# Kernel tuning notes

Hardware: AMD Instinct MI355X
Metric: run time of the kernel (lower is better)

## Reference

```python
import jax, jax.numpy as jnp
import numpy as np

N, E, G = 20000, 100000, 32
HID, HEADS, HC = 64, 8, 64  # hidden, heads, per-head channels (PyG: out_channels per head)
L, K = 3, 4


def setup_inputs() -> dict:
    key = jax.random.key(0)
    ks = jax.random.split(key, 20)
    rn = lambda k, s, sc=0.05: jax.random.normal(k, s, jnp.float32) * sc
    HO = HEADS * HC  # 512
    return {
        "x": jax.random.uniform(ks[0], (N, 7), jnp.float32),
        "edge_attr": jax.random.normal(ks[1], (E, 4), jnp.float32),
        "means": jax.random.normal(ks[2], (K, 8), jnp.float32),
        "log_stds": jnp.zeros((K, 8), jnp.float32),
        "sp_W": rn(ks[3], (K, HID), 0.3), "sp_b": jnp.zeros((HID,), jnp.float32),
        "ne_W": rn(ks[4], (7, HID), 0.3), "ne_b": jnp.zeros((HID,), jnp.float32),
        "ee_W": rn(ks[5], (4, HID), 0.3), "ee_b": jnp.zeros((HID,), jnp.float32),
        "Wq": rn(ks[6], (L, HID, HO)), "bq": jnp.zeros((L, HO), jnp.float32),
        "Wk": rn(ks[7], (L, HID, HO)), "bk": jnp.zeros((L, HO), jnp.float32),
        "Wv": rn(ks[8], (L, HID, HO)), "bv": jnp.zeros((L, HO), jnp.float32),
        "We": rn(ks[9], (L, HID, HO)), "be": jnp.zeros((L, HO), jnp.float32),
        "Ws": rn(ks[10], (L, HID, HID)), "bs": jnp.zeros((L, HID), jnp.float32),
        "eu_W": rn(ks[11], (L, 3 * HID, HID)), "eu_b": jnp.zeros((L, HID), jnp.float32),
        "rW1": rn(ks[12], (2 * HID, HID)), "rb1": jnp.zeros((HID,), jnp.float32),
        "rW2": rn(ks[13], (HID, HID)), "rb2": jnp.zeros((HID,), jnp.float32),
        "rW3": rn(ks[14], (HID, 2)), "rb3": jnp.zeros((2,), jnp.float32),
        "edge_index": jax.random.randint(ks[15], (2, E), 0, N, jnp.int32),
        "batch": jnp.sort(jax.random.randint(ks[16], (N,), 0, G, jnp.int32)),
        "num_graphs": G,
    }


def reference(x, edge_attr, means, log_stds, sp_W, sp_b, ne_W, ne_b, ee_W, ee_b,
              Wq, bq, Wk, bk, Wv, bv, We, be, Ws, bs, eu_W, eu_b,
              rW1, rb1, rW2, rb2, rW3, rb3, edge_index, batch, num_graphs):
    n = x.shape[0]
    src, dst = edge_index[0], edge_index[1]

    # ---- SpatialGaussianEncoder (dropout is identity in eval) ----
    p = x[:, :4]
    sl, sr = p[src, :2], p[src, 2:4]
    dl, dr = p[dst, :2], p[dst, 2:4]
    rel = jnp.stack([dl - sl, dl - sr, dr - sl, dr - sr], axis=1)  # [E,4,2]
    dist = jnp.linalg.norm(rel, axis=-1)                           # [E,4]
    ang = jnp.arctan2(rel[..., 1], rel[..., 0])                    # [E,4]
    u = jnp.stack([dist, ang], axis=-1).reshape(-1, 8)             # [E,8] (d,a)x4
    std = jnp.exp(log_stds) + 1e-6                                 # [K,8]
    z = (u[:, None, :] - means[None]) / std[None]                  # [E,K,8]
    w = jnp.exp(-0.5 * jnp.sum(z * z, axis=-1))                    # [E,K]
    sp = jax.nn.relu(w @ sp_W + sp_b)                              # [E,HID]

    h = jax.nn.relu(x @ ne_W + ne_b)                               # [N,HID]
    ea = jax.nn.relu(edge_attr @ ee_W + ee_b) + sp                 # [E,HID]

    scale = 1.0 / float(np.sqrt(HC))
    for l in range(L):
        # PyG TransformerConv(hidden, hidden, heads=8, edge_dim=hidden, concat=False)
        q = (h @ Wq[l] + bq[l]).reshape(n, HEADS, HC)
        k = (h @ Wk[l] + bk[l]).reshape(n, HEADS, HC)
        v = (h @ Wv[l] + bv[l]).reshape(n, HEADS, HC)
        e = (ea @ We[l] + be[l]).reshape(-1, HEADS, HC)
        kj = k[src] + e                                            # [E,H,C]
        alpha = jnp.einsum('ehc,ehc->eh', q[dst], kj) * scale      # [E,H]
        m = jax.ops.segment_max(alpha, dst, num_segments=n)
        ex = jnp.exp(alpha - m[dst])
        den = jax.ops.segment_sum(ex, dst, num_segments=n)
        a = ex / (den[dst] + 1e-16)                                # scatter-softmax over dst
        msg = a[:, :, None] * (v[src] + e)                         # [E,H,C]
        out = jax.ops.segment_sum(msg, dst, num_segments=n).mean(axis=1)  # concat=False -> head mean
        h = jax.nn.relu(out + h @ Ws[l] + bs[l])                   # skip (root_weight) + F.relu
        ef = jnp.concatenate([h[src], h[dst], ea], axis=1)         # [E,3*HID]
        ea = jax.nn.relu(ef @ eu_W[l] + eu_b[l])

    # ---- per-graph masked-mean pooling == segment mean ----
    cn = jnp.maximum(jax.ops.segment_sum(jnp.ones((n,), x.dtype), batch, num_segments=num_graphs), 1.0)
    node_pool = jax.ops.segment_sum(h, batch, num_segments=num_graphs) / cn[:, None]
    eb = batch[src]
    ce = jnp.maximum(jax.ops.segment_sum(jnp.ones((src.shape[0],), x.dtype), eb, num_segments=num_graphs), 1.0)
    edge_pool = jax.ops.segment_sum(ea, eb, num_segments=num_graphs) / ce[:, None]
    g = jnp.concatenate([node_pool, edge_pool], axis=1)            # [G,2*HID]

    h1 = jax.nn.relu(g @ rW1 + rb1)
    h2 = jax.nn.relu(h1 @ rW2 + rb2)
    return jnp.tanh(h2 @ rW3 + rb3)                                # [G,2]
```

## Files before the change

### kernel.cpp

```cpp
#include <hip/hip_runtime.h>
#include <hip/hip_bf16.h>
#include <cstdint>
#include <cstddef>



__global__ void __launch_bounds__(256) k_node_embed(
    const float* __restrict__ x, const float* __restrict__ neW, const float* __restrict__ neb,
    float* __restrict__ h, int N)
{
    int idx = blockIdx.x * 256 + threadIdx.x;
    int n = idx >> 6, c = idx & 63;
    if (n >= N) return;
    float acc = neb[c];
    #pragma unroll
    for (int j = 0; j < 7; ++j) acc += x[(size_t)n * 7 + j] * neW[j * 64 + c];
    h[(size_t)n * 64 + c] = fmaxf(acc, 0.f);
}

__global__ void __launch_bounds__(256) k_edge_w(
    const float* __restrict__ x,
    const float* __restrict__ means, const float* __restrict__ log_stds,
    const int* __restrict__ src, const int* __restrict__ dst,
    float* __restrict__ wbuf, int E)
{
    int e = blockIdx.x * 256 + threadIdx.x;
    if (e >= E) return;
    int s = src[e], d = dst[e];
    const float* ps = x + (size_t)s * 7;
    const float* pd = x + (size_t)d * 7;
    float slx = ps[0], sly = ps[1], srx = ps[2], sry = ps[3];
    float dlx = pd[0], dly = pd[1], drx = pd[2], dry = pd[3];
    float u[8];
    float rx, ry;
    rx = dlx - slx; ry = dly - sly; u[0] = sqrtf(rx*rx + ry*ry); u[1] = atan2f(ry, rx);
    rx = dlx - srx; ry = dly - sry; u[2] = sqrtf(rx*rx + ry*ry); u[3] = atan2f(ry, rx);
    rx = drx - slx; ry = dry - sly; u[4] = sqrtf(rx*rx + ry*ry); u[5] = atan2f(ry, rx);
    rx = drx - srx; ry = dry - sry; u[6] = sqrtf(rx*rx + ry*ry); u[7] = atan2f(ry, rx);
    #pragma unroll
    for (int kk = 0; kk < 4; ++kk) {
        float ssum = 0.f;
        #pragma unroll
        for (int dd = 0; dd < 8; ++dd) {
            float stdv = expf(log_stds[kk*8+dd]) + 1e-6f;
            float z = (u[dd] - means[kk*8+dd]) / stdv;
            ssum += z * z;
        }
        wbuf[(size_t)e*4 + kk] = expf(-0.5f * ssum);
    }
}

__global__ void __launch_bounds__(256) k_edge_ea(
    const float* __restrict__ edge_attr, const float* __restrict__ wbuf,
    const float* __restrict__ spW, const float* __restrict__ spb,
    const float* __restrict__ eeW, const float* __restrict__ eeb,
    float* __restrict__ ea, int E)
{
    int idx = blockIdx.x * 256 + threadIdx.x;
    int e = idx >> 6, c = idx & 63;
    if (e >= E) return;
    float acce = eeb[c];
    #pragma unroll
    for (int j = 0; j < 4; ++j) acce += edge_attr[(size_t)e*4 + j] * eeW[j*64 + c];
    float accs = spb[c];
    #pragma unroll
    for (int j = 0; j < 4; ++j) accs += wbuf[(size_t)e*4 + j] * spW[j*64 + c];
    ea[(size_t)e*64 + c] = fmaxf(acce, 0.f) + fmaxf(accs, 0.f);
}


__global__ void __launch_bounds__(256) k_hist(
    const int* __restrict__ dst, int* __restrict__ deg, int E)
{
    int e = blockIdx.x * 256 + threadIdx.x;
    if (e < E) atomicAdd(deg + dst[e], 1);
}

__global__ void __launch_bounds__(1024) k_scan(
    const int* __restrict__ deg, int* __restrict__ ptr, int* __restrict__ headw, int N)
{
    __shared__ int part[1024];
    int t = threadIdx.x;
    int per = (N + 1023) / 1024;
    int s = 0;
    for (int i = 0; i < per; ++i) { int idx = t*per + i; if (idx < N) s += deg[idx]; }
    part[t] = s;
    __syncthreads();
    for (int off = 1; off < 1024; off <<= 1) {
        int v = (t >= off) ? part[t - off] : 0;
        __syncthreads();
        part[t] += v;
        __syncthreads();
    }
    int base = (t > 0) ? part[t - 1] : 0;
    for (int i = 0; i < per; ++i) {
        int idx = t*per + i;
        if (idx < N) { ptr[idx] = base; headw[idx] = base; base += deg[idx]; }
    }
    if (t == 1023) ptr[N] = part[1023];
}

__global__ void __launch_bounds__(256) k_scatter(
    const int* __restrict__ dst, const int* __restrict__ src, const int* __restrict__ batch,
    int* __restrict__ headw, int2* __restrict__ ipair, int* __restrict__ ieb, int E)
{
    int e = blockIdx.x * 256 + threadIdx.x;
    if (e < E) {
        int s = src[e];
        int pos = atomicAdd(headw + dst[e], 1);
        ipair[pos] = make_int2(s, e);
        ieb[e] = batch[s];
    }
}


__global__ void __launch_bounds__(256) k_wprod_all(
    const float* __restrict__ Wq, const float* __restrict__ bq,
    const float* __restrict__ Wk, const float* __restrict__ We,
    float* __restrict__ Mk, float* __restrict__ Me,
    float* __restrict__ bqk, float* __restrict__ bqe)
{
    int h = blockIdx.x;
    int which = blockIdx.y;
    int l = blockIdx.z;
    const float* Wq_l = Wq + (size_t)l * 64 * 512;
    const float* bq_l = bq + (size_t)l * 512;
    const float* Wx_l = (which ? We : Wk) + (size_t)l * 64 * 512;
    float* M  = (which ? Me : Mk) + (size_t)l * 64 * 512;
    float* bM = (which ? bqe : bqk) + (size_t)l * 512;
    __shared__ float wq_s[65][64];
    __shared__ float wx_s[64][65];
    int tid = threadIdx.x;
    for (int i = tid; i < 4096; i += 256) {
        int r = i >> 6, c2 = i & 63;
        wq_s[r][c2] = Wq_l[(size_t)r*512 + h*64 + c2];
        wx_s[r][c2] = Wx_l[(size_t)r*512 + h*64 + c2];
    }
    if (tid < 64) wq_s[64][tid] = bq_l[h*64 + tid];
    __syncthreads();
    int j = tid & 63, cg = tid >> 6;
    for (int c = cg*16; c < cg*16 + 16; ++c) {
        float s = 0.f;
        #pragma unroll 8
        for (int c2 = 0; c2 < 64; ++c2) s += wq_s[c][c2] * wx_s[j][c2];
        M[(size_t)c*512 + h*64 + j] = s;
    }
    if (tid < 64) {
        float s = 0.f;
        #pragma unroll 8
        for (int c2 = 0; c2 < 64; ++c2) s += wq_s[64][c2] * wx_s[tid][c2];
        bM[h*64 + tid] = s;
    }
}

__global__ void __launch_bounds__(64) k_wqb_all(
    const float* __restrict__ Wq, const float* __restrict__ bq,
    const float* __restrict__ bk, const float* __restrict__ be,
    float* __restrict__ wqb, float* __restrict__ cb)
{
    int l = blockIdx.x;
    const float* Wq_l = Wq + (size_t)l * 64 * 512;
    const float* bq_l = bq + (size_t)l * 512;
    const float* bk_l = bk + (size_t)l * 512;
    const float* be_l = be + (size_t)l * 512;
    float* wqb_l = wqb + (size_t)l * 512;
    float* cb_l  = cb + (size_t)l * 8;
    int c = threadIdx.x;
    for (int h = 0; h < 8; ++h) {
        float s = 0.f;
        for (int c2 = 0; c2 < 64; ++c2)
            s += Wq_l[(size_t)c*512 + h*64 + c2] * (bk_l[h*64+c2] + be_l[h*64+c2]);
        wqb_l[c*8 + h] = s;
    }
    if (c < 8) {
        float s = 0.f;
        for (int c2 = 0; c2 < 64; ++c2)
            s += bq_l[c*64 + c2] * (bk_l[c*64+c2] + be_l[c*64+c2]);
        cb_l[c] = s;
    }
}


__global__ void __launch_bounds__(256) k_proj16(
    const float* __restrict__ h,
    const float* __restrict__ Mk, const float* __restrict__ bqk, float* __restrict__ qk,
    const float* __restrict__ Me, const float* __restrict__ bqe, float* __restrict__ qe2,
    int N)
{
    __shared__ float As[64][132];
    __shared__ __align__(16) float Wt[64][64];
    int tid = threadIdx.x;
    int y = blockIdx.y;
    int which = y >> 3, yb = y & 7;
    const float* W    = which ? Me : Mk;
    const float* bias = (which ? bqe : bqk) + yb * 64;
    float* Y          = which ? qe2 : qk;
    int n0 = blockIdx.x * 128;
    {
        int rt = tid & 127;
        int n = n0 + rt;
        int jh = (tid >> 7) * 32;
        if (n < N) {
            const float* ap = h + (size_t)n*64;
            #pragma unroll
            for (int j4 = 0; j4 < 8; ++j4) {
                int j = jh + j4 * 4;
                float4 a = *(const float4*)(ap + j);
                As[j+0][rt] = a.x; As[j+1][rt] = a.y;
                As[j+2][rt] = a.z; As[j+3][rt] = a.w;
            }
        } else {
            #pragma unroll
            for (int j4 = 0; j4 < 8; ++j4) {
                int j = jh + j4 * 4;
                As[j+0][rt] = 0.f; As[j+1][rt] = 0.f;
                As[j+2][rt] = 0.f; As[j+3][rt] = 0.f;
            }
        }
        #pragma unroll
        for (int i = 0; i < 4; ++i) {
            int idx = tid + i * 256;
            int j = idx >> 4, c4 = (idx & 15) * 4;
            *(float4*)&Wt[j][c4] = *(const float4*)(W + (size_t)j*512 + yb*64 + c4);
        }
    }
    __syncthreads();
    int wv = tid >> 6, lane = tid & 63;
    int rg = lane >> 3, cg = lane & 7;
    int c0 = cg * 8;
    int rbase = wv * 32 + rg * 4;
    float acc[4][8];
    float4 b0 = *(const float4*)(bias + c0);
    float4 b1 = *(const float4*)(bias + c0 + 4);
    #pragma unroll
    for (int t = 0; t < 4; ++t) {
        acc[t][0]=b0.x; acc[t][1]=b0.y; acc[t][2]=b0.z; acc[t][3]=b0.w;
        acc[t][4]=b1.x; acc[t][5]=b1.y; acc[t][6]=b1.z; acc[t][7]=b1.w;
    }
    #pragma unroll 4
    for (int j = 0; j < 64; ++j) {
        float4 av = *(const float4*)&As[j][rbase];
        float4 w0 = *(const float4*)&Wt[j][c0];
        float4 w1 = *(const float4*)&Wt[j][c0 + 4];
        acc[0][0] += av.x*w0.x; acc[0][1] += av.x*w0.y; acc[0][2] += av.x*w0.z; acc[0][3] += av.x*w0.w;
        acc[0][4] += av.x*w1.x; acc[0][5] += av.x*w1.y; acc[0][6] += av.x*w1.z; acc[0][7] += av.x*w1.w;
        acc[1][0] += av.y*w0.x; acc[1][1] += av.y*w0.y; acc[1][2] += av.y*w0.z; acc[1][3] += av.y*w0.w;
        acc[1][4] += av.y*w1.x; acc[1][5] += av.y*w1.y; acc[1][6] += av.y*w1.z; acc[1][7] += av.y*w1.w;
        acc[2][0] += av.z*w0.x; acc[2][1] += av.z*w0.y; acc[2][2] += av.z*w0.z; acc[2][3] += av.z*w0.w;
        acc[2][4] += av.z*w1.x; acc[2][5] += av.z*w1.y; acc[2][6] += av.z*w1.z; acc[2][7] += av.z*w1.w;
        acc[3][0] += av.w*w0.x; acc[3][1] += av.w*w0.y; acc[3][2] += av.w*w0.z; acc[3][3] += av.w*w0.w;
        acc[3][4] += av.w*w1.x; acc[3][5] += av.w*w1.y; acc[3][6] += av.w*w1.z; acc[3][7] += av.w*w1.w;
    }
    #pragma unroll
    for (int t = 0; t < 4; ++t) {
        int n = n0 + rbase + t;
        if (n < N) {
            float4 o0 = {acc[t][0],acc[t][1],acc[t][2],acc[t][3]};
            float4 o1 = {acc[t][4],acc[t][5],acc[t][6],acc[t][7]};
            *(float4*)(Y + (size_t)n*512 + yb*64 + c0)     = o0;
            *(float4*)(Y + (size_t)n*512 + yb*64 + c0 + 4) = o1;
        }
    }
}


__global__ void __launch_bounds__(256) k_attn_fused(
    const float* __restrict__ qk, const float* __restrict__ qe2,
    const float* __restrict__ wqb, const float* __restrict__ cb,
    const float* __restrict__ ea, const float* __restrict__ hbuf,
    const int* __restrict__ ptr, const int2* __restrict__ ipair,
    float* __restrict__ hagg, float* __restrict__ tbuf, float* __restrict__ sbuf, int N)
{
    int wv = threadIdx.x >> 6, lane = threadIdx.x & 63;
    int n = blockIdx.x * 4 + wv;
    if (n >= N) return;
    int h = lane >> 3, p = lane & 7;
    int b = ptr[n], e_ = ptr[n + 1];
    int deg = e_ - b;
    const float4* xp = (const float4*)(qk + (size_t)n*512 + lane*8);
    float4 x0 = xp[0], x1 = xp[1];
    const float4* gp = (const float4*)(qe2 + (size_t)n*512 + lane*8);
    float4 g0 = gp[0], g1 = gp[1];
    const float4* hdp = (const float4*)(hbuf + (size_t)n*64 + p*8);
    float4 hd0 = hdp[0], hd1 = hdp[1];
    float qbh = hd0.x*wqb[(p*8+0)*8+h] + hd0.y*wqb[(p*8+1)*8+h]
              + hd0.z*wqb[(p*8+2)*8+h] + hd0.w*wqb[(p*8+3)*8+h]
              + hd1.x*wqb[(p*8+4)*8+h] + hd1.y*wqb[(p*8+5)*8+h]
              + hd1.z*wqb[(p*8+6)*8+h] + hd1.w*wqb[(p*8+7)*8+h];
    qbh += __shfl_xor(qbh, 1);
    qbh += __shfl_xor(qbh, 2);
    qbh += __shfl_xor(qbh, 4);
    qbh += cb[h];
    float m = -3.4e38f, den = 0.f;
    float hacc[8], tacc[8];
    #pragma unroll
    for (int i = 0; i < 8; ++i) { hacc[i] = 0.f; tacc[i] = 0.f; }
    for (int base = 0; base < deg; base += 64) {
        int cnt = deg - base; if (cnt > 64) cnt = 64;
        int2 myp = (lane < cnt) ? ipair[b + base + lane] : make_int2(0, 0);
        int s0i = __shfl(myp.x, 0), e0i = __shfl(myp.y, 0);
        const float4* hp = (const float4*)(hbuf + (size_t)s0i*64 + p*8);
        const float4* ap = (const float4*)(ea + (size_t)e0i*64 + p*8);
        float4 h0 = hp[0], h1 = hp[1];
        float4 a0 = ap[0], a1 = ap[1];
        for (int i = 0; i < cnt; ++i) {
            float4 h0c = h0, h1c = h1, a0c = a0, a1c = a1;
            if (i + 1 < cnt) {
                int sn = __shfl(myp.x, i + 1), en = __shfl(myp.y, i + 1);
                const float4* hpn = (const float4*)(hbuf + (size_t)sn*64 + p*8);
                const float4* apn = (const float4*)(ea + (size_t)en*64 + p*8);
                h0 = hpn[0]; h1 = hpn[1]; a0 = apn[0]; a1 = apn[1];
            }
            float t = x0.x*h0c.x + x0.y*h0c.y + x0.z*h0c.z + x0.w*h0c.w
                    + x1.x*h1c.x + x1.y*h1c.y + x1.z*h1c.z + x1.w*h1c.w
                    + g0.x*a0c.x + g0.y*a0c.y + g0.z*a0c.z + g0.w*a0c.w
                    + g1.x*a1c.x + g1.y*a1c.y + g1.z*a1c.z + g1.w*a1c.w;
            t += __shfl_xor(t, 1);
            t += __shfl_xor(t, 2);
            t += __shfl_xor(t, 4);
            float al = 0.125f * (t + qbh);
            float mn = fmaxf(m, al);
            float r = expf(m - mn);
            float w = expf(al - mn);
            den = den * r + w;
            m = mn;
            hacc[0] = hacc[0]*r + w*h0c.x; hacc[1] = hacc[1]*r + w*h0c.y;
            hacc[2] = hacc[2]*r + w*h0c.z; hacc[3] = hacc[3]*r + w*h0c.w;
            hacc[4] = hacc[4]*r + w*h1c.x; hacc[5] = hacc[5]*r + w*h1c.y;
            hacc[6] = hacc[6]*r + w*h1c.z; hacc[7] = hacc[7]*r + w*h1c.w;
            tacc[0] = tacc[0]*r + w*a0c.x; tacc[1] = tacc[1]*r + w*a0c.y;
            tacc[2] = tacc[2]*r + w*a0c.z; tacc[3] = tacc[3]*r + w*a0c.w;
            tacc[4] = tacc[4]*r + w*a1c.x; tacc[5] = tacc[5]*r + w*a1c.y;
            tacc[6] = tacc[6]*r + w*a1c.z; tacc[7] = tacc[7]*r + w*a1c.w;
        }
    }
    float inv = 0.125f / (den + 1e-16f);
    float4 o;
    o = {hacc[0]*inv,hacc[1]*inv,hacc[2]*inv,hacc[3]*inv};
    *(float4*)(hagg + (size_t)n*512 + lane*8)     = o;
    o = {hacc[4]*inv,hacc[5]*inv,hacc[6]*inv,hacc[7]*inv};
    *(float4*)(hagg + (size_t)n*512 + lane*8 + 4) = o;
    o = {tacc[0]*inv,tacc[1]*inv,tacc[2]*inv,tacc[3]*inv};
    *(float4*)(tbuf + (size_t)n*512 + lane*8)     = o;
    o = {tacc[4]*inv,tacc[5]*inv,tacc[6]*inv,tacc[7]*inv};
    *(float4*)(tbuf + (size_t)n*512 + lane*8 + 4) = o;
    if (p == 0) sbuf[(size_t)n*8 + h] = den * inv;
}

__global__ void __launch_bounds__(256) k_nf_gemm2(
    const float* __restrict__ tbuf, const float* __restrict__ hagg,
    const float* __restrict__ We, const float* __restrict__ Wv,
    float* __restrict__ pbuf, int N)
{
    __shared__ float As[64][132];
    __shared__ __align__(16) float Wt[64][64];
    int tid = threadIdx.x;
    int y = blockIdx.y;
    int n0 = blockIdx.x * 128;
    int wv = tid >> 6, lane = tid & 63;
    int rg = lane >> 3, cg = lane & 7;
    int c0 = cg * 8;
    int rbase = wv * 32 + rg * 4;
    float acc[4][8];
    #pragma unroll
    for (int t = 0; t < 4; ++t)
        #pragma unroll
        for (int i = 0; i < 8; ++i) acc[t][i] = 0.f;
    #pragma unroll
    for (int round = 0; round < 2; ++round) {
        const float* A = round ? hagg : tbuf;
        const float* W = round ? Wv : We;
        if (round) __syncthreads();
        {
            int rt = tid & 127;
            int n = n0 + rt;
            int jh = (tid >> 7) * 32;
            if (n < N) {
                const float* ap = A + (size_t)n*512 + y*64;
                #pragma unroll
                for (int j4 = 0; j4 < 8; ++j4) {
                    int j = jh + j4 * 4;
                    float4 a = *(const float4*)(ap + j);
                    As[j+0][rt] = a.x; As[j+1][rt] = a.y;
                    As[j+2][rt] = a.z; As[j+3][rt] = a.w;
                }
            } else {
                #pragma unroll
                for (int j4 = 0; j4 < 8; ++j4) {
                    int j = jh + j4 * 4;
                    As[j+0][rt] = 0.f; As[j+1][rt] = 0.f;
                    As[j+2][rt] = 0.f; As[j+3][rt] = 0.f;
                }
            }
            #pragma unroll
            for (int i = 0; i < 4; ++i) {
                int idx = tid + i * 256;
                int j = idx >> 4, c4 = (idx & 15) * 4;
                *(float4*)&Wt[j][c4] = *(const float4*)(W + (size_t)j*512 + y*64 + c4);
            }
        }
        __syncthreads();
        #pragma unroll 4
        for (int j = 0; j < 64; ++j) {
            float4 av = *(const float4*)&As[j][rbase];
            float4 w0 = *(const float4*)&Wt[j][c0];
            float4 w1 = *(const float4*)&Wt[j][c0 + 4];
            acc[0][0] += av.x*w0.x; acc[0][1] += av.x*w0.y; acc[0][2] += av.x*w0.z; acc[0][3] += av.x*w0.w;
            acc[0][4] += av.x*w1.x; acc[0][5] += av.x*w1.y; acc[0][6] += av.x*w1.z; acc[0][7] += av.x*w1.w;
            acc[1][0] += av.y*w0.x; acc[1][1] += av.y*w0.y; acc[1][2] += av.y*w0.z; acc[1][3] += av.y*w0.w;
            acc[1][4] += av.y*w1.x; acc[1][5] += av.y*w1.y; acc[1][6] += av.y*w1.z; acc[1][7] += av.y*w1.w;
            acc[2][0] += av.z*w0.x; acc[2][1] += av.z*w0.y; acc[2][2] += av.z*w0.z; acc[2][3] += av.z*w0.w;
            acc[2][4] += av.z*w1.x; acc[2][5] += av.z*w1.y; acc[2][6] += av.z*w1.z; acc[2][7] += av.z*w1.w;
            acc[3][0] += av.w*w0.x; acc[3][1] += av.w*w0.y; acc[3][2] += av.w*w0.z; acc[3][3] += av.w*w0.w;
            acc[3][4] += av.w*w1.x; acc[3][5] += av.w*w1.y; acc[3][6] += av.w*w1.z; acc[3][7] += av.w*w1.w;
        }
    }
    float* out = pbuf + (size_t)y * N * 64;
    #pragma unroll
    for (int t = 0; t < 4; ++t) {
        int n = n0 + rbase + t;
        if (n < N) {
            float4 o0 = {acc[t][0],acc[t][1],acc[t][2],acc[t][3]};
            float4 o1 = {acc[t][4],acc[t][5],acc[t][6],acc[t][7]};
            *(float4*)(out + (size_t)n*64 + c0)     = o0;
            *(float4*)(out + (size_t)n*64 + c0 + 4) = o1;
        }
    }
}

__global__ void __launch_bounds__(256) k_nf_reduce2(
    const float* __restrict__ pbuf, const float* __restrict__ hin,
    const float* __restrict__ sbuf, const float* __restrict__ Ws,
    const float* __restrict__ be, const float* __restrict__ bv,
    const float* __restrict__ bs, float* __restrict__ hnext, int N)
{
    int idx = blockIdx.x * 256 + threadIdx.x;
    int n = idx >> 6, cc = idx & 63;
    if (n >= N) return;
    float a = bs[cc];
    #pragma unroll
    for (int y = 0; y < 8; ++y) a += pbuf[(size_t)y*N*64 + (size_t)n*64 + cc];
    float hv = hin[(size_t)n*64 + cc];
    #pragma unroll 8
    for (int j = 0; j < 64; ++j) a += __shfl(hv, j) * Ws[(size_t)j*64 + cc];
    #pragma unroll
    for (int h = 0; h < 8; ++h)
        a += sbuf[(size_t)n*8 + h] * (be[h*64 + cc] + bv[h*64 + cc]);
    hnext[(size_t)n*64 + cc] = fmaxf(a, 0.f);
}

__global__ void __launch_bounds__(256) k_eu_pre(
    const float* __restrict__ h, const float* __restrict__ euW,
    float* __restrict__ hw, int N)
{
    __shared__ float As[64][132];
    __shared__ __align__(16) float Wt[64][64];
    int tid = threadIdx.x;
    int y = blockIdx.y;
    int n0 = blockIdx.x * 128;
    {
        int rt = tid & 127;
        int n = n0 + rt;
        int jh = (tid >> 7) * 32;
        if (n < N) {
            const float* ap = h + (size_t)n*64;
            #pragma unroll
            for (int j4 = 0; j4 < 8; ++j4) {
                int j = jh + j4 * 4;
                float4 a = *(const float4*)(ap + j);
                As[j+0][rt] = a.x; As[j+1][rt] = a.y;
                As[j+2][rt] = a.z; As[j+3][rt] = a.w;
            }
        } else {
            #pragma unroll
            for (int j4 = 0; j4 < 8; ++j4) {
                int j = jh + j4 * 4;
                As[j+0][rt] = 0.f; As[j+1][rt] = 0.f;
                As[j+2][rt] = 0.f; As[j+3][rt] = 0.f;
            }
        }
        #pragma unroll
        for (int i = 0; i < 4; ++i) {
            int idx = tid + i * 256;
            *(float4*)&Wt[idx >> 4][(idx & 15) * 4] =
                *(const float4*)(euW + (size_t)y*4096 + idx * 4);
        }
    }
    __syncthreads();
    int wv = tid >> 6, lane = tid & 63;
    int rg = lane >> 3, cg = lane & 7;
    int c0 = cg * 8;
    int rbase = wv * 32 + rg * 4;
    float acc[4][8];
    #pragma unroll
    for (int t = 0; t < 4; ++t)
        #pragma unroll
        for (int i = 0; i < 8; ++i) acc[t][i] = 0.f;
    #pragma unroll 4
    for (int j = 0; j < 64; ++j) {
        float4 av = *(const float4*)&As[j][rbase];
        float4 w0 = *(const float4*)&Wt[j][c0];
        float4 w1 = *(const float4*)&Wt[j][c0 + 4];
        acc[0][0] += av.x*w0.x; acc[0][1] += av.x*w0.y; acc[0][2] += av.x*w0.z; acc[0][3] += av.x*w0.w;
        acc[0][4] += av.x*w1.x; acc[0][5] += av.x*w1.y; acc[0][6] += av.x*w1.z; acc[0][7] += av.x*w1.w;
        acc[1][0] += av.y*w0.x; acc[1][1] += av.y*w0.y; acc[1][2] += av.y*w0.z; acc[1][3] += av.y*w0.w;
        acc[1][4] += av.y*w1.x; acc[1][5] += av.y*w1.y; acc[1][6] += av.y*w1.z; acc[1][7] += av.y*w1.w;
        acc[2][0] += av.z*w0.x; acc[2][1] += av.z*w0.y; acc[2][2] += av.z*w0.z; acc[2][3] += av.z*w0.w;
        acc[2][4] += av.z*w1.x; acc[2][5] += av.z*w1.y; acc[2][6] += av.z*w1.z; acc[2][7] += av.z*w1.w;
        acc[3][0] += av.w*w0.x; acc[3][1] += av.w*w0.y; acc[3][2] += av.w*w0.z; acc[3][3] += av.w*w0.w;
        acc[3][4] += av.w*w1.x; acc[3][5] += av.w*w1.y; acc[3][6] += av.w*w1.z; acc[3][7] += av.w*w1.w;
    }
    #pragma unroll
    for (int t = 0; t < 4; ++t) {
        int n = n0 + rbase + t;
        if (n < N) {
            float4 o0 = {acc[t][0],acc[t][1],acc[t][2],acc[t][3]};
            float4 o1 = {acc[t][4],acc[t][5],acc[t][6],acc[t][7]};
            *(float4*)(hw + (size_t)n*128 + y*64 + c0)     = o0;
            *(float4*)(hw + (size_t)n*128 + y*64 + c0 + 4) = o1;
        }
    }
}

__global__ void __launch_bounds__(256) k_edge_update2(
    const float* __restrict__ hw, const float* __restrict__ ea,
    const float* __restrict__ euW2, const float* __restrict__ eub,
    const int* __restrict__ src, const int* __restrict__ dst,
    float* __restrict__ ea2, int E)
{
    __shared__ float As[64][132];
    __shared__ __align__(16) float Wt[64][64];
    __shared__ int sid[128], did[128];
    int tid = threadIdx.x;
    int e0 = blockIdx.x * 128;
    if (tid < 128) {
        int e = e0 + tid; if (e >= E) e = E - 1;
        sid[tid] = src[e]; did[tid] = dst[e];
    }
    {
        int et = tid & 127;
        int e = e0 + et; if (e >= E) e = E - 1;
        const float* ap = ea + (size_t)e * 64;
        int jh = (tid >> 7) * 32;
        #pragma unroll
        for (int j4 = 0; j4 < 8; ++j4) {
            int j = jh + j4 * 4;
            float4 a = *(const float4*)(ap + j);
            As[j+0][et] = a.x; As[j+1][et] = a.y;
            As[j+2][et] = a.z; As[j+3][et] = a.w;
        }
        #pragma unroll
        for (int i = 0; i < 4; ++i) {
            int idx = tid + i * 256;
            *(float4*)&Wt[idx >> 4][(idx & 15) * 4] = *(const float4*)(euW2 + idx * 4);
        }
    }
    __syncthreads();
    int wv = tid >> 6, lane = tid & 63;
    int rg = lane >> 3, cg = lane & 7;
    int c0 = cg * 8;
    int rbase = wv * 32 + rg * 4;
    float acc[4][8];
    float4 b0 = *(const float4*)(eub + c0);
    float4 b1 = *(const float4*)(eub + c0 + 4);
    #pragma unroll
    for (int t = 0; t < 4; ++t) {
        acc[t][0]=b0.x; acc[t][1]=b0.y; acc[t][2]=b0.z; acc[t][3]=b0.w;
        acc[t][4]=b1.x; acc[t][5]=b1.y; acc[t][6]=b1.z; acc[t][7]=b1.w;
    }
    #pragma unroll 4
    for (int j = 0; j < 64; ++j) {
        float4 av = *(const float4*)&As[j][rbase];
        float4 w0 = *(const float4*)&Wt[j][c0];
        float4 w1 = *(const float4*)&Wt[j][c0 + 4];
        acc[0][0] += av.x*w0.x; acc[0][1] += av.x*w0.y; acc[0][2] += av.x*w0.z; acc[0][3] += av.x*w0.w;
        acc[0][4] += av.x*w1.x; acc[0][5] += av.x*w1.y; acc[0][6] += av.x*w1.z; acc[0][7] += av.x*w1.w;
        acc[1][0] += av.y*w0.x; acc[1][1] += av.y*w0.y; acc[1][2] += av.y*w0.z; acc[1][3] += av.y*w0.w;
        acc[1][4] += av.y*w1.x; acc[1][5] += av.y*w1.y; acc[1][6] += av.y*w1.z; acc[1][7] += av.y*w1.w;
        acc[2][0] += av.z*w0.x; acc[2][1] += av.z*w0.y; acc[2][2] += av.z*w0.z; acc[2][3] += av.z*w0.w;
        acc[2][4] += av.z*w1.x; acc[2][5] += av.z*w1.y; acc[2][6] += av.z*w1.z; acc[2][7] += av.z*w1.w;
        acc[3][0] += av.w*w0.x; acc[3][1] += av.w*w0.y; acc[3][2] += av.w*w0.z; acc[3][3] += av.w*w0.w;
        acc[3][4] += av.w*w1.x; acc[3][5] += av.w*w1.y; acc[3][6] += av.w*w1.z; acc[3][7] += av.w*w1.w;
    }
    #pragma unroll
    for (int t = 0; t < 4; ++t) {
        int e = e0 + rbase + t;
        if (e < E) {
            int s = sid[rbase + t], d = did[rbase + t];
            const float4* sp = (const float4*)(hw + (size_t)s*128 + c0);
            const float4* dp = (const float4*)(hw + (size_t)d*128 + 64 + c0);
            float4 s0 = sp[0], s1 = sp[1];
            float4 d0 = dp[0], d1 = dp[1];
            float4 o0 = {fmaxf(acc[t][0]+s0.x+d0.x,0.f), fmaxf(acc[t][1]+s0.y+d0.y,0.f),
                         fmaxf(acc[t][2]+s0.z+d0.z,0.f), fmaxf(acc[t][3]+s0.w+d0.w,0.f)};
            float4 o1 = {fmaxf(acc[t][4]+s1.x+d1.x,0.f), fmaxf(acc[t][5]+s1.y+d1.y,0.f),
                         fmaxf(acc[t][6]+s1.z+d1.z,0.f), fmaxf(acc[t][7]+s1.w+d1.w,0.f)};
            *(float4*)(ea2 + (size_t)e*64 + c0)     = o0;
            *(float4*)(ea2 + (size_t)e*64 + c0 + 4) = o1;
        }
    }
}


__global__ void __launch_bounds__(64) k_node_pool(
    const float* __restrict__ h, const int* __restrict__ batch,
    float* __restrict__ npool, float* __restrict__ cn, int N)
{
    int lane = threadIdx.x;
    int n0 = blockIdx.x * 64;
    float acc = 0.f; int cur = -1; int run = 0;
    for (int i = 0; i < 64; ++i) {
        int n = n0 + i;
        if (n >= N) break;
        int b = batch[n];
        if (b != cur) {
            if (cur >= 0) {
                atomicAdd(npool + (size_t)cur*64 + lane, acc);
                if (lane == 0) atomicAdd(cn + cur, (float)run);
            }
            cur = b; acc = 0.f; run = 0;
        }
        acc += h[(size_t)n*64 + lane];
        ++run;
    }
    if (cur >= 0) {
        atomicAdd(npool + (size_t)cur*64 + lane, acc);
        if (lane == 0) atomicAdd(cn + cur, (float)run);
    }
}

__global__ void __launch_bounds__(256) k_edge_pool2(
    const float* __restrict__ ea, const int* __restrict__ ieb,
    float* __restrict__ rep, int E)
{
    __shared__ float pool_s[32][64];
    __shared__ float cnt_s[32];
    int tid = threadIdx.x;
    for (int i = tid; i < 2048; i += 256) ((float*)pool_s)[i] = 0.f;
    if (tid < 32) cnt_s[tid] = 0.f;
    __syncthreads();
    int wv = tid >> 6, lane = tid & 63;
    int base = blockIdx.x * 64 + wv * 16;
    int b16[16]; float v16[16];
    #pragma unroll
    for (int u = 0; u < 16; ++u) {
        int e = base + u;
        bool ok = (e < E);
        b16[u] = ok ? ieb[e] : -1;
        v16[u] = ok ? ea[(size_t)e*64 + lane] : 0.f;
    }
    #pragma unroll
    for (int u = 0; u < 16; ++u) {
        if (b16[u] >= 0) {
            atomicAdd(&pool_s[b16[u]][lane], v16[u]);
            if (lane == 0) atomicAdd(&cnt_s[b16[u]], 1.f);
        }
    }
    __syncthreads();
    float* myrep = rep + (size_t)(blockIdx.x & 7) * 2080;
    for (int i = tid; i < 2048; i += 256) atomicAdd(myrep + i, ((float*)pool_s)[i]);
    if (tid < 32) atomicAdd(myrep + 2048 + tid, cnt_s[tid]);
}

__global__ void __launch_bounds__(256) k_pool_merge(
    const float* __restrict__ rep, float* __restrict__ epool, float* __restrict__ ce)
{
    int i = blockIdx.x * 256 + threadIdx.x;
    if (i < 2080) {
        float s = 0.f;
        #pragma unroll
        for (int r = 0; r < 8; ++r) s += rep[(size_t)r*2080 + i];
        if (i < 2048) epool[i] = s; else ce[i - 2048] = s;
    }
}

__global__ void __launch_bounds__(64) k_head_mlp(
    const float* __restrict__ npool, const float* __restrict__ epool,
    const float* __restrict__ cn, const float* __restrict__ ce,
    const float* __restrict__ rW1, const float* __restrict__ rb1,
    const float* __restrict__ rW2, const float* __restrict__ rb2,
    const float* __restrict__ rW3, const float* __restrict__ rb3,
    float* __restrict__ out)
{
    __shared__ float g[128];
    __shared__ float h1[64];
    __shared__ float h2[64];
    int b = blockIdx.x, lane = threadIdx.x;
    float cnv = fmaxf(cn[b], 1.f), cev = fmaxf(ce[b], 1.f);
    g[lane]      = npool[(size_t)b*64 + lane] / cnv;
    g[64 + lane] = epool[(size_t)b*64 + lane] / cev;
    __syncthreads();
    float acc = rb1[lane];
    #pragma unroll 4
    for (int j = 0; j < 128; ++j) acc += g[j] * rW1[j*64 + lane];
    h1[lane] = fmaxf(acc, 0.f);
    __syncthreads();
    acc = rb2[lane];
    #pragma unroll 4
    for (int j = 0; j < 64; ++j) acc += h1[j] * rW2[j*64 + lane];
    h2[lane] = fmaxf(acc, 0.f);
    __syncthreads();
    if (lane < 2) {
        float o = rb3[lane];
        for (int j = 0; j < 64; ++j) o += h2[j] * rW3[j*2 + lane];
        out[b*2 + lane] = tanhf(o);
    }
}


extern "C" void kernel_launch(void* const* d_in, const int* in_sizes, int n_in,
                              void* d_out, int out_size, void* d_ws, size_t ws_size,
                              hipStream_t stream)
{
    const float* x         = (const float*)d_in[0];
    const float* edge_attr = (const float*)d_in[1];
    const float* means     = (const float*)d_in[2];
    const float* log_stds  = (const float*)d_in[3];
    const float* spW       = (const float*)d_in[4];
    const float* spb       = (const float*)d_in[5];
    const float* neW       = (const float*)d_in[6];
    const float* neb       = (const float*)d_in[7];
    const float* eeW       = (const float*)d_in[8];
    const float* eeb       = (const float*)d_in[9];
    const float* Wq        = (const float*)d_in[10];
    const float* bq        = (const float*)d_in[11];
    const float* Wk        = (const float*)d_in[12];
    const float* bk        = (const float*)d_in[13];
    const float* Wv        = (const float*)d_in[14];
    const float* bv        = (const float*)d_in[15];
    const float* We        = (const float*)d_in[16];
    const float* be        = (const float*)d_in[17];
    const float* Ws        = (const float*)d_in[18];
    const float* bs        = (const float*)d_in[19];
    const float* euW       = (const float*)d_in[20];
    const float* eub       = (const float*)d_in[21];
    const float* rW1       = (const float*)d_in[22];
    const float* rb1       = (const float*)d_in[23];
    const float* rW2       = (const float*)d_in[24];
    const float* rb2       = (const float*)d_in[25];
    const float* rW3       = (const float*)d_in[26];
    const float* rb3       = (const float*)d_in[27];
    const int* eidx        = (const int*)d_in[28];
    const int* batch       = (const int*)d_in[29];

    int N = in_sizes[0] / 7;
    int E = in_sizes[1] / 4;
    const int G = 32;
    const int* srcp = eidx;
    const int* dstp = eidx + E;

    float* ws = (float*)d_ws;
    size_t fl = 0;
    float* hA    = ws + fl; fl += (size_t)N * 64;
    float* hB    = ws + fl; fl += (size_t)N * 64;
    float* eaA   = ws + fl; fl += (size_t)E * 64;
    float* eaB   = ws + fl; fl += (size_t)E * 64;
    float* B1    = ws + fl; fl += (size_t)N * 512;
    float* B2    = ws + fl; fl += (size_t)N * 512;
    float* B3    = ws + fl; fl += (size_t)N * 512;
    float* alpha = ws + fl; fl += (size_t)E * 8;
    float* sbuf  = ws + fl; fl += (size_t)N * 8;
    float* npool = ws + fl; fl += (size_t)G * 64;
    float* epool = ws + fl; fl += (size_t)G * 64;
    float* cn    = ws + fl; fl += G;
    float* ce    = ws + fl; fl += G;
    float* Mk3   = ws + fl; fl += 3 * 64 * 512;
    float* Me3   = ws + fl; fl += 3 * 64 * 512;
    float* bqk3  = ws + fl; fl += 3 * 512;
    float* bqe3  = ws + fl; fl += 3 * 512;
    float* wqb3  = ws + fl; fl += 3 * 512;
    float* cb3   = ws + fl; fl += 24;
    float* rep   = ws + fl; fl += 8 * 2080;
    int* ideg  = (int*)(ws + fl); fl += (size_t)N;
    int* ihead = (int*)(ws + fl); fl += (size_t)N;
    int2* ipair = (int2*)(ws + fl); fl += (size_t)E * 2;
    int* ieb   = (int*)(ws + fl); fl += (size_t)E;
    int* iptr  = (int*)(ws + fl); fl += (size_t)N + 1;

    float* wbuf = alpha;

    hipMemsetAsync(npool, 0, (size_t)(G * 130) * sizeof(float), stream);
    hipMemsetAsync(rep, 0, (size_t)(8 * 2080) * sizeof(float), stream);
    hipMemsetAsync(ideg, 0, (size_t)N * sizeof(int), stream);

    k_node_embed<<<(N * 64 + 255) / 256, 256, 0, stream>>>(x, neW, neb, hA, N);
    k_edge_w<<<(E + 255) / 256, 256, 0, stream>>>(x, means, log_stds, srcp, dstp, wbuf, E);
    k_edge_ea<<<((size_t)E * 64 + 255) / 256, 256, 0, stream>>>(edge_attr, wbuf,
                                                                spW, spb, eeW, eeb, eaA, E);
    k_hist<<<(E + 255) / 256, 256, 0, stream>>>(dstp, ideg, E);
    k_scan<<<1, 1024, 0, stream>>>(ideg, iptr, ihead, N);
    k_scatter<<<(E + 255) / 256, 256, 0, stream>>>(dstp, srcp, batch, ihead, ipair, ieb, E);
    k_wprod_all<<<dim3(8, 2, 3), 256, 0, stream>>>(Wq, bq, Wk, We, Mk3, Me3, bqk3, bqe3);
    k_wqb_all<<<3, 64, 0, stream>>>(Wq, bq, bk, be, wqb3, cb3);

    float* hcur = hA;  float* hnext = hB;
    float* eacur = eaA; float* eanext = eaB;
    for (int l = 0; l < 3; ++l) {
        const float* Wv_l = Wv + (size_t)l * 64 * 512;
        const float* We_l = We + (size_t)l * 64 * 512;
        const float* bv_l = bv + (size_t)l * 512;
        const float* be_l = be + (size_t)l * 512;
        const float* euW_l = euW + (size_t)l * 192 * 64;

        k_proj16<<<dim3((N + 127) / 128, 16), 256, 0, stream>>>(
            hcur,
            Mk3 + (size_t)l * 32768, bqk3 + (size_t)l * 512, B1,
            Me3 + (size_t)l * 32768, bqe3 + (size_t)l * 512, B2, N);

        k_attn_fused<<<(N + 3) / 4, 256, 0, stream>>>(B1, B2,
                                                      wqb3 + (size_t)l * 512,
                                                      cb3 + (size_t)l * 8,
                                                      eacur, hcur,
                                                      iptr, ipair,
                                                      B1 , B2 , sbuf, N);
        k_nf_gemm2<<<dim3((N + 127) / 128, 8), 256, 0, stream>>>(B2, B1, We_l, Wv_l, B3, N);
        k_nf_reduce2<<<((size_t)N * 64 + 255) / 256, 256, 0, stream>>>(B3, hcur, sbuf,
                                                                       Ws + (size_t)l * 64 * 64,
                                                                       be_l, bv_l,
                                                                       bs + (size_t)l * 64,
                                                                       hnext, N);
        k_eu_pre<<<dim3((N + 127) / 128, 2), 256, 0, stream>>>(hnext, euW_l, B3, N);
        k_edge_update2<<<(E + 127) / 128, 256, 0, stream>>>(B3, eacur, euW_l + 2 * 4096,
                                                            eub + (size_t)l * 64,
                                                            srcp, dstp, eanext, E);
        float* t1 = hcur; hcur = hnext; hnext = t1;
        float* t2 = eacur; eacur = eanext; eanext = t2;
    }

    k_node_pool<<<(N + 63) / 64, 64, 0, stream>>>(hcur, batch, npool, cn, N);
    k_edge_pool2<<<(E + 63) / 64, 256, 0, stream>>>(eacur, ieb, rep, E);
    k_pool_merge<<<9, 256, 0, stream>>>(rep, epool, ce);
    k_head_mlp<<<G, 64, 0, stream>>>(npool, epool, cn, ce, rW1, rb1, rW2, rb2, rW3, rb3,
                                     (float*)d_out);
}
```

Measured before the change: 719.4 us.

## Store edge features in dst-sorted CSR order to make attention reads contiguous

```diff
diff --git a/kernel.cpp b/kernel.cpp
--- a/kernel.cpp
+++ b/kernel.cpp
@@ -21,12 +21,12 @@
 __global__ void __launch_bounds__(256) k_edge_w(
     const float* __restrict__ x,
     const float* __restrict__ means, const float* __restrict__ log_stds,
-    const int* __restrict__ src, const int* __restrict__ dst,
+    const int2* __restrict__ ipair, const int* __restrict__ idst,
     float* __restrict__ wbuf, int E)
 {
-    int e = blockIdx.x * 256 + threadIdx.x;
-    if (e >= E) return;
-    int s = src[e], d = dst[e];
+    int slot = blockIdx.x * 256 + threadIdx.x;
+    if (slot >= E) return;
+    int s = ipair[slot].x, d = idst[slot];
     const float* ps = x + (size_t)s * 7;
     const float* pd = x + (size_t)d * 7;
     float slx = ps[0], sly = ps[1], srx = ps[2], sry = ps[3];
@@ -46,26 +46,28 @@
             float z = (u[dd] - means[kk*8+dd]) / stdv;
             ssum += z * z;
         }
-        wbuf[(size_t)e*4 + kk] = expf(-0.5f * ssum);
+        wbuf[(size_t)slot*4 + kk] = expf(-0.5f * ssum);
     }
 }
 
 __global__ void __launch_bounds__(256) k_edge_ea(
     const float* __restrict__ edge_attr, const float* __restrict__ wbuf,
+    const int2* __restrict__ ipair,
     const float* __restrict__ spW, const float* __restrict__ spb,
     const float* __restrict__ eeW, const float* __restrict__ eeb,
     float* __restrict__ ea, int E)
 {
     int idx = blockIdx.x * 256 + threadIdx.x;
-    int e = idx >> 6, c = idx & 63;
-    if (e >= E) return;
+    int slot = idx >> 6, c = idx & 63;
+    if (slot >= E) return;
+    int e = ipair[slot].y;
     float acce = eeb[c];
     #pragma unroll
     for (int j = 0; j < 4; ++j) acce += edge_attr[(size_t)e*4 + j] * eeW[j*64 + c];
     float accs = spb[c];
     #pragma unroll
-    for (int j = 0; j < 4; ++j) accs += wbuf[(size_t)e*4 + j] * spW[j*64 + c];
-    ea[(size_t)e*64 + c] = fmaxf(acce, 0.f) + fmaxf(accs, 0.f);
+    for (int j = 0; j < 4; ++j) accs += wbuf[(size_t)slot*4 + j] * spW[j*64 + c];
+    ea[(size_t)slot*64 + c] = fmaxf(acce, 0.f) + fmaxf(accs, 0.f);
 }
 
 
@@ -102,14 +104,17 @@
 
 __global__ void __launch_bounds__(256) k_scatter(
     const int* __restrict__ dst, const int* __restrict__ src, const int* __restrict__ batch,
-    int* __restrict__ headw, int2* __restrict__ ipair, int* __restrict__ ieb, int E)
+    int* __restrict__ headw, int2* __restrict__ ipair, int* __restrict__ idst,
+    int* __restrict__ iebs, int E)
 {
     int e = blockIdx.x * 256 + threadIdx.x;
     if (e < E) {
         int s = src[e];
-        int pos = atomicAdd(headw + dst[e], 1);
+        int d = dst[e];
+        int pos = atomicAdd(headw + d, 1);
         ipair[pos] = make_int2(s, e);
-        ieb[e] = batch[s];
+        idst[pos] = d;
+        iebs[pos] = batch[s];
     }
 }
 
@@ -298,17 +303,17 @@
     for (int base = 0; base < deg; base += 64) {
         int cnt = deg - base; if (cnt > 64) cnt = 64;
         int2 myp = (lane < cnt) ? ipair[b + base + lane] : make_int2(0, 0);
-        int s0i = __shfl(myp.x, 0), e0i = __shfl(myp.y, 0);
+        int s0i = __shfl(myp.x, 0);
         const float4* hp = (const float4*)(hbuf + (size_t)s0i*64 + p*8);
-        const float4* ap = (const float4*)(ea + (size_t)e0i*64 + p*8);
+        const float4* ap = (const float4*)(ea + (size_t)(b + base)*64 + p*8);
         float4 h0 = hp[0], h1 = hp[1];
         float4 a0 = ap[0], a1 = ap[1];
         for (int i = 0; i < cnt; ++i) {
             float4 h0c = h0, h1c = h1, a0c = a0, a1c = a1;
             if (i + 1 < cnt) {
-                int sn = __shfl(myp.x, i + 1), en = __shfl(myp.y, i + 1);
+                int sn = __shfl(myp.x, i + 1);
                 const float4* hpn = (const float4*)(hbuf + (size_t)sn*64 + p*8);
-                const float4* apn = (const float4*)(ea + (size_t)en*64 + p*8);
+                const float4* apn = (const float4*)(ea + (size_t)(b + base + i + 1)*64 + p*8);
                 h0 = hpn[0]; h1 = hpn[1]; a0 = apn[0]; a1 = apn[1];
             }
             float t = x0.x*h0c.x + x0.y*h0c.y + x0.z*h0c.z + x0.w*h0c.w
@@ -525,7 +530,7 @@
 __global__ void __launch_bounds__(256) k_edge_update2(
     const float* __restrict__ hw, const float* __restrict__ ea,
     const float* __restrict__ euW2, const float* __restrict__ eub,
-    const int* __restrict__ src, const int* __restrict__ dst,
+    const int2* __restrict__ ipair, const int* __restrict__ idst,
     float* __restrict__ ea2, int E)
 {
     __shared__ float As[64][132];
@@ -534,13 +539,13 @@
     int tid = threadIdx.x;
     int e0 = blockIdx.x * 128;
     if (tid < 128) {
-        int e = e0 + tid; if (e >= E) e = E - 1;
-        sid[tid] = src[e]; did[tid] = dst[e];
+        int slot = e0 + tid; if (slot >= E) slot = E - 1;
+        sid[tid] = ipair[slot].x; did[tid] = idst[slot];
     }
     {
         int et = tid & 127;
-        int e = e0 + et; if (e >= E) e = E - 1;
-        const float* ap = ea + (size_t)e * 64;
+        int slot = e0 + et; if (slot >= E) slot = E - 1;
+        const float* ap = ea + (size_t)slot * 64;
         int jh = (tid >> 7) * 32;
         #pragma unroll
         for (int j4 = 0; j4 < 8; ++j4) {
@@ -584,8 +589,8 @@
     }
     #pragma unroll
     for (int t = 0; t < 4; ++t) {
-        int e = e0 + rbase + t;
-        if (e < E) {
+        int slot = e0 + rbase + t;
+        if (slot < E) {
             int s = sid[rbase + t], d = did[rbase + t];
             const float4* sp = (const float4*)(hw + (size_t)s*128 + c0);
             const float4* dp = (const float4*)(hw + (size_t)d*128 + 64 + c0);
@@ -595,8 +600,8 @@
                          fmaxf(acc[t][2]+s0.z+d0.z,0.f), fmaxf(acc[t][3]+s0.w+d0.w,0.f)};
             float4 o1 = {fmaxf(acc[t][4]+s1.x+d1.x,0.f), fmaxf(acc[t][5]+s1.y+d1.y,0.f),
                          fmaxf(acc[t][6]+s1.z+d1.z,0.f), fmaxf(acc[t][7]+s1.w+d1.w,0.f)};
-            *(float4*)(ea2 + (size_t)e*64 + c0)     = o0;
-            *(float4*)(ea2 + (size_t)e*64 + c0 + 4) = o1;
+            *(float4*)(ea2 + (size_t)slot*64 + c0)     = o0;
+            *(float4*)(ea2 + (size_t)slot*64 + c0 + 4) = o1;
         }
     }
 }
@@ -630,7 +635,7 @@
 }
 
 __global__ void __launch_bounds__(256) k_edge_pool2(
-    const float* __restrict__ ea, const int* __restrict__ ieb,
+    const float* __restrict__ ea, const int* __restrict__ iebs,
     float* __restrict__ rep, int E)
 {
     __shared__ float pool_s[32][64];
@@ -644,10 +649,10 @@
     int b16[16]; float v16[16];
     #pragma unroll
     for (int u = 0; u < 16; ++u) {
-        int e = base + u;
-        bool ok = (e < E);
-        b16[u] = ok ? ieb[e] : -1;
-        v16[u] = ok ? ea[(size_t)e*64 + lane] : 0.f;
+        int slot = base + u;
+        bool ok = (slot < E);
+        b16[u] = ok ? iebs[slot] : -1;
+        v16[u] = ok ? ea[(size_t)slot*64 + lane] : 0.f;
     }
     #pragma unroll
     for (int u = 0; u < 16; ++u) {
@@ -774,7 +779,8 @@
     int* ideg  = (int*)(ws + fl); fl += (size_t)N;
     int* ihead = (int*)(ws + fl); fl += (size_t)N;
     int2* ipair = (int2*)(ws + fl); fl += (size_t)E * 2;
-    int* ieb   = (int*)(ws + fl); fl += (size_t)E;
+    int* idst  = (int*)(ws + fl); fl += (size_t)E;
+    int* iebs  = (int*)(ws + fl); fl += (size_t)E;
     int* iptr  = (int*)(ws + fl); fl += (size_t)N + 1;
 
     float* wbuf = alpha;
@@ -784,12 +790,13 @@
     hipMemsetAsync(ideg, 0, (size_t)N * sizeof(int), stream);
 
     k_node_embed<<<(N * 64 + 255) / 256, 256, 0, stream>>>(x, neW, neb, hA, N);
-    k_edge_w<<<(E + 255) / 256, 256, 0, stream>>>(x, means, log_stds, srcp, dstp, wbuf, E);
-    k_edge_ea<<<((size_t)E * 64 + 255) / 256, 256, 0, stream>>>(edge_attr, wbuf,
-                                                                spW, spb, eeW, eeb, eaA, E);
     k_hist<<<(E + 255) / 256, 256, 0, stream>>>(dstp, ideg, E);
     k_scan<<<1, 1024, 0, stream>>>(ideg, iptr, ihead, N);
-    k_scatter<<<(E + 255) / 256, 256, 0, stream>>>(dstp, srcp, batch, ihead, ipair, ieb, E);
+    k_scatter<<<(E + 255) / 256, 256, 0, stream>>>(dstp, srcp, batch, ihead,
+                                                   ipair, idst, iebs, E);
+    k_edge_w<<<(E + 255) / 256, 256, 0, stream>>>(x, means, log_stds, ipair, idst, wbuf, E);
+    k_edge_ea<<<((size_t)E * 64 + 255) / 256, 256, 0, stream>>>(edge_attr, wbuf, ipair,
+                                                                spW, spb, eeW, eeb, eaA, E);
     k_wprod_all<<<dim3(8, 2, 3), 256, 0, stream>>>(Wq, bq, Wk, We, Mk3, Me3, bqk3, bqe3);
     k_wqb_all<<<3, 64, 0, stream>>>(Wq, bq, bk, be, wqb3, cb3);
 
@@ -822,13 +829,13 @@
         k_eu_pre<<<dim3((N + 127) / 128, 2), 256, 0, stream>>>(hnext, euW_l, B3, N);
         k_edge_update2<<<(E + 127) / 128, 256, 0, stream>>>(B3, eacur, euW_l + 2 * 4096,
                                                             eub + (size_t)l * 64,
-                                                            srcp, dstp, eanext, E);
+                                                            ipair, idst, eanext, E);
         float* t1 = hcur; hcur = hnext; hnext = t1;
         float* t2 = eacur; eacur = eanext; eanext = t2;
     }
 
     k_node_pool<<<(N + 63) / 64, 64, 0, stream>>>(hcur, batch, npool, cn, N);
-    k_edge_pool2<<<(E + 63) / 64, 256, 0, stream>>>(eacur, ieb, rep, E);
+    k_edge_pool2<<<(E + 63) / 64, 256, 0, stream>>>(eacur, iebs, rep, E);
     k_pool_merge<<<9, 256, 0, stream>>>(rep, epool, ce);
     k_head_mlp<<<G, 64, 0, stream>>>(npool, epool, cn, ce, rW1, rb1, rW2, rb2, rW3, rb3,
                                      (float*)d_out);
```

Measured after the change: 716.8 us, median of 2. No clear change (-0.4%).
